# Kernel optimization log

Hardware: AMD Instinct MI355X
Metric: run time of the kernel (lower is better)

Reference implementation:

```python
import jax, jax.numpy as jnp
import numpy as np

K = 6

def _diag_indices(H, W):
    # stable argsort of anti-diagonal index i+j over row-major flattening
    i = np.arange(H)[:, None]
    j = np.arange(W)[None, :]
    order = np.argsort((i + j).ravel(), kind='stable')
    return order, np.argsort(order, kind='stable')

def _selective_scan(u, delta, A, Bs, Cs, D, delta_bias):
    # u, delta: (B,K,D,L); A: (K,D,N); Bs,Cs: (B,K,N,L); D,delta_bias: (K,D)
    delta = jax.nn.softplus(delta + delta_bias[None, :, :, None])
    dA = jnp.exp(jnp.einsum('bkdl,kdn->lbkdn', delta, A))          # (L,B,K,D,N)
    dBu = jnp.einsum('bkdl,bknl,bkdl->lbkdn', delta, Bs, u)         # (L,B,K,D,N)
    Cl = jnp.moveaxis(Cs, -1, 0)                                    # (L,B,K,N)
    x0 = jnp.zeros(dA.shape[1:], dA.dtype)
    def step(x, inp):
        dA_t, dBu_t, C_t = inp
        x = dA_t * x + dBu_t
        y = jnp.einsum('bkdn,bkn->bkd', x, C_t)
        return x, y
    _, ys = jax.lax.scan(step, x0, (dA, dBu, Cl))
    y = jnp.moveaxis(ys, 0, -1)                                     # (B,K,D,L)
    return y + u * D[None, :, :, None]

def reference(x, W_in, conv_w, conv_b, x_proj_w, dt_w, dt_b, A_logs, Ds, ln_g, ln_b, W_out):
    B, H, W, C = x.shape
    L = H * W
    di = dt_w.shape[1]
    dt_rank = dt_w.shape[2]
    N = A_logs.shape[1]
    # in_proj (no bias) and split
    xz = jnp.einsum('bhwc,oc->bhwo', x, W_in)
    xx, z = jnp.split(xz, 2, axis=-1)
    # depthwise conv 3x3, SAME padding, + bias, SiLU
    xc = jnp.transpose(xx, (0, 3, 1, 2))                            # (B,di,H,W)
    xc = jax.lax.conv_general_dilated(xc, conv_w, (1, 1), 'SAME',
            feature_group_count=di, dimension_numbers=('NCHW', 'OIHW', 'NCHW'))
    xc = jax.nn.silu(xc + conv_b[None, :, None, None])
    # build 6 scan orderings
    x_flat = xc.reshape(B, di, L)
    x_t = jnp.transpose(xc, (0, 1, 3, 2)).reshape(B, di, L)
    x_hwwh = jnp.stack([x_flat, x_t], axis=1)                       # (B,2,di,L)
    xs4 = jnp.concatenate([x_hwwh, x_hwwh[..., ::-1]], axis=1)      # (B,4,di,L)
    x_invhh = jnp.flip(xc, axis=-1).reshape(B, di, L)               # flip W only
    x_hh = jnp.stack([x_flat, x_invhh], axis=1)                     # (B,2,di,L)
    diag_idx, rev_idx = _diag_indices(H, W)
    xs = jnp.concatenate([xs4, x_hh[..., diag_idx]], axis=1)        # (B,6,di,L)
    # projections
    x_dbl = jnp.einsum('bkdl,kcd->bkcl', xs, x_proj_w)
    dts, Bs, Cs = jnp.split(x_dbl, [dt_rank, dt_rank + N], axis=2)
    dts = jnp.einsum('bkrl,kdr->bkdl', dts, dt_w)
    A = -jnp.exp(A_logs).reshape(K, di, N)
    out_y = _selective_scan(xs, dts, A, Bs, Cs, Ds.reshape(K, di), dt_b)
    # undo the 6 orderings
    inv_y = out_y[:, 2:4][..., ::-1]
    wh_y = jnp.transpose(out_y[:, 1].reshape(B, di, W, H), (0, 1, 3, 2)).reshape(B, di, L)
    invwh_y = jnp.transpose(inv_y[:, 1].reshape(B, di, W, H), (0, 1, 3, 2)).reshape(B, di, L)
    transhh = out_y[:, 4:6][..., rev_idx]
    invhh = transhh[:, 1][..., ::-1]
    y = out_y[:, 0] + inv_y[:, 0] + wh_y + invwh_y + transhh[:, 0] + invhh  # (B,di,L)
    y = jnp.transpose(y, (0, 2, 1)).reshape(B, H, W, di)
    # LayerNorm (eps=1e-5)
    mu = y.mean(-1, keepdims=True)
    var = ((y - mu) ** 2).mean(-1, keepdims=True)
    y = (y - mu) * jax.lax.rsqrt(var + 1e-5) * ln_g + ln_b
    y = y * jax.nn.silu(z)
    return jnp.einsum('bhwd,od->bhwo', y, W_out)

def setup_inputs():
    key = jax.random.key(0)
    ks = jax.random.split(key, 8)
    d_model, di, N, dt_rank = 64, 128, 16, 4
    x = jax.random.normal(ks[0], (1, 64, 64, d_model), jnp.float32)
    W_in = jax.random.normal(ks[1], (2 * di, d_model), jnp.float32) * d_model ** -0.5
    conv_w = jax.random.normal(ks[2], (di, 1, 3, 3), jnp.float32) / 3.0
    conv_b = jnp.zeros((di,), jnp.float32)
    x_proj_w = jax.random.normal(ks[3], (K, dt_rank + 2 * N, di), jnp.float32) * di ** -0.5
    s = dt_rank ** -0.5
    dt_w = jax.random.uniform(ks[4], (K, di, dt_rank), jnp.float32, -s, s)
    dt = jnp.exp(jax.random.uniform(ks[5], (K, di), jnp.float32)
                 * (np.log(0.1) - np.log(0.001)) + np.log(0.001))
    dt = jnp.clip(dt, 1e-4)
    dt_b = dt + jnp.log(-jnp.expm1(-dt))
    A_logs = jnp.log(jnp.tile(jnp.arange(1, N + 1, dtype=jnp.float32)[None, :], (K * di, 1)))
    Ds = jnp.ones((K * di,), jnp.float32)
    ln_g = jnp.ones((di,), jnp.float32)
    ln_b = jnp.zeros((di,), jnp.float32)
    W_out = jax.random.normal(ks[6], (d_model, di), jnp.float32) * di ** -0.5
    return {"x": x, "W_in": W_in, "conv_w": conv_w, "conv_b": conv_b,
            "x_proj_w": x_proj_w, "dt_w": dt_w, "dt_b": dt_b, "A_logs": A_logs,
            "Ds": Ds, "ln_g": ln_g, "ln_b": ln_b, "W_out": W_out}
```

## Files before the change

kernel.cpp:

```cpp
#include <hip/hip_runtime.h>
#include <math.h>

#define L    4096
#define DI   128
#define NS   16
#define KK   6
#define DTR  4
#define CM   64
#define NC   256
#define CH   (L/NC)

__device__ __forceinline__ float softplus_f(float x){
    return x > 20.f ? x : __logf(1.f + __expf(x));
}
__device__ __forceinline__ float silu_f(float x){
    return x / (1.f + __expf(-x));
}

__device__ __forceinline__ int rankp(int p){
    int h = p >> 6, w = p & 63, s = h + w;
    int imin = s > 63 ? s - 63 : 0;
    int off = (s < 64) ? (s*(s+1))/2 : 4096 - ((127-s)*(128-s))/2;
    return off + (h - imin);
}

__device__ __forceinline__ int perm_in(int k, int l, const int* __restrict__ diag){
    switch(k){
        case 0: return l;
        case 1: return ((l&63)<<6) | (l>>6);
        case 2: return (L-1) - l;
        case 3: { int m = (L-1)-l; return ((m&63)<<6) | (m>>6); }
        case 4: return diag[l];
        default: return diag[l] ^ 63;
    }
}

__global__ __launch_bounds__(256) void k_init(const float* __restrict__ W_in,
                                              const float* __restrict__ W_out,
                                              int* __restrict__ diag_idx,
                                              float* __restrict__ WI4,
                                              float* __restrict__ WO4){
    int t = blockIdx.x*256 + threadIdx.x;
    diag_idx[rankp(t)] = t;
    {
        int d4 = t >> 8, o = t & 255;
        float4 v = make_float4(W_in[(size_t)o*CM + d4*4+0], W_in[(size_t)o*CM + d4*4+1],
                               W_in[(size_t)o*CM + d4*4+2], W_in[(size_t)o*CM + d4*4+3]);
        ((float4*)WI4)[d4*256 + o] = v;
    }
    if(t < 2048){
        int d4 = t >> 6, o = t & 63;
        float4 v = make_float4(W_out[(size_t)o*DI + d4*4+0], W_out[(size_t)o*DI + d4*4+1],
                               W_out[(size_t)o*DI + d4*4+2], W_out[(size_t)o*DI + d4*4+3]);
        ((float4*)WO4)[d4*64 + o] = v;
    }
}

__global__ __launch_bounds__(256) void k_inproj(const float* __restrict__ x,
                                                const float* __restrict__ WI4,
                                                float* __restrict__ xx_t,
                                                float* __restrict__ sz){
    int pb = blockIdx.x * 8;
    int o  = threadIdx.x;
    __shared__ float xr[8][CM];
    if(o < 128) ((float4*)&xr[0][0])[o] = ((const float4*)(x + (size_t)pb*CM))[o];
    float4 w[16];
    const float4* W4 = (const float4*)WI4;
    #pragma unroll
    for(int q=0;q<16;q++) w[q] = W4[q*256 + o];
    __syncthreads();
    float acc[8];
    #pragma unroll
    for(int pi=0;pi<8;pi++) acc[pi] = 0.f;
    #pragma unroll
    for(int q=0;q<16;q++){
        float4 wv = w[q];
        #pragma unroll
        for(int pi=0;pi<8;pi++){
            float4 xv = *((const float4*)&xr[pi][q*4]);
            acc[pi] += wv.x*xv.x + wv.y*xv.y + wv.z*xv.z + wv.w*xv.w;
        }
    }
    #pragma unroll
    for(int pi=0;pi<8;pi++){
        int p = pb + pi;
        if(o < DI) xx_t[(size_t)p*DI + o] = acc[pi];
        else       sz[(size_t)p*DI + (o-DI)] = silu_f(acc[pi]);
    }
}

__global__ __launch_bounds__(256) void k_conv(const float* __restrict__ xx_t,
                                              const float* __restrict__ cw,
                                              const float* __restrict__ cb,
                                              float* __restrict__ xc_t){
    int idx = blockIdx.x*256 + threadIdx.x;
    int d = idx & 127, p = idx >> 7;
    int h = p >> 6, w = p & 63;
    float acc = cb[d];
    #pragma unroll
    for(int dh=-1; dh<=1; dh++){
        int hh = h+dh; if(hh < 0 || hh >= 64) continue;
        #pragma unroll
        for(int dw=-1; dw<=1; dw++){
            int ww = w+dw; if(ww < 0 || ww >= 64) continue;
            acc += cw[d*9 + (dh+1)*3+(dw+1)] * xx_t[(size_t)(hh*64+ww)*DI + d];
        }
    }
    xc_t[idx] = silu_f(acc);
}

#define XT_S 132
__global__ __launch_bounds__(256) void k_proj(const float* __restrict__ xc_t,
                                              const float* __restrict__ xpw,
                                              const int* __restrict__ diag,
                                              float* __restrict__ dts,
                                              float* __restrict__ BT,
                                              float* __restrict__ CT){
    int k  = blockIdx.x >> 6;
    int l0 = (blockIdx.x & 63) * 64;
    int t  = threadIdx.x;
    __shared__ float xt[64*XT_S];
    #pragma unroll
    for(int q=0;q<8;q++){
        int lin = q*256 + t;
        int row = lin >> 5, col4 = lin & 31;
        int p = perm_in(k, l0+row, diag);
        float4 v = ((const float4*)(xc_t + (size_t)p*DI))[col4];
        *((float4*)(xt + row*XT_S + col4*4)) = v;
    }
    __syncthreads();
    int l = t & 63, c0 = (t>>6)*9;
    const float* xr = xt + l*XT_S;
    float acc[9];
    #pragma unroll
    for(int j=0;j<9;j++) acc[j] = 0.f;
    const float4* wbase = (const float4*)(xpw + (size_t)k*36*DI);
    for(int dd4=0; dd4<32; dd4++){
        float4 xv = *((const float4*)(xr + dd4*4));
        #pragma unroll
        for(int j=0;j<9;j++){
            float4 wv = wbase[(c0+j)*32 + dd4];
            acc[j] += wv.x*xv.x + wv.y*xv.y + wv.z*xv.z + wv.w*xv.w;
        }
    }
    #pragma unroll
    for(int j=0;j<9;j++){
        int c = c0 + j;
        if(c < 4)        dts[((size_t)k*4 + c)*L + l0 + l] = acc[j];
        else if(c < 20)  BT[((size_t)k*L + l0 + l)*NS + (c-4)]  = acc[j];
        else             CT[((size_t)k*L + l0 + l)*NS + (c-20)] = acc[j];
    }
}

__global__ __launch_bounds__(128) void k_scan1(const float* __restrict__ xc_t,
                                               const float* __restrict__ dts,
                                               const float* __restrict__ BT,
                                               const float* __restrict__ dtw,
                                               const float* __restrict__ dtb,
                                               const float* __restrict__ A_logs,
                                               const int* __restrict__ diag,
                                               float* __restrict__ apb,
                                               float* __restrict__ xlb){
    int bk = blockIdx.x;
    int k = bk >> 8, cc = bk & (NC-1);
    int d = threadIdx.x;
    int l0 = cc*CH;

    __shared__ float Bt[CH*NS];
    __shared__ float dtt[4*CH];
    __shared__ int   pt[CH];

    if(d < 64) ((float4*)Bt)[d] = ((const float4*)(BT + ((size_t)k*L + l0)*NS))[d];
    else { int j = d-64; int r = j>>4, i = j&15;
           dtt[j] = dts[((size_t)k*4 + r)*L + l0 + i]; }
    if(d < CH) pt[d] = perm_in(k, l0+d, diag);
    __syncthreads();

    float u[CH];
    #pragma unroll
    for(int i=0;i<CH;i++) u[i] = xc_t[(size_t)pt[i]*DI + d];

    float4 w4 = ((const float4*)dtw)[(size_t)k*DI + d];
    float  bb = dtb[k*DI + d];
    float A[NS];
    {
        const float4* ar = (const float4*)(A_logs + ((size_t)k*DI + d)*NS);
        #pragma unroll
        for(int q=0;q<4;q++){
            float4 a4 = ar[q];
            A[q*4+0] = -__expf(a4.x); A[q*4+1] = -__expf(a4.y);
            A[q*4+2] = -__expf(a4.z); A[q*4+3] = -__expf(a4.w);
        }
    }
    float x[NS], ap[NS];
    #pragma unroll
    for(int n=0;n<NS;n++){ x[n] = 0.f; ap[n] = 1.f; }

    #pragma unroll
    for(int i=0;i<CH;i++){
        float dv = bb + w4.x*dtt[i] + w4.y*dtt[CH+i] + w4.z*dtt[2*CH+i] + w4.w*dtt[3*CH+i];
        float delta = softplus_f(dv);
        float du = delta*u[i];
        const float* Bi = Bt + i*NS;
        #pragma unroll
        for(int n=0;n<NS;n++){
            float da = __expf(delta*A[n]);
            x[n] = da*x[n] + du*Bi[n];
            ap[n] *= da;
        }
    }
    float* apd = apb + ((size_t)bk*DI + d)*NS;
    float* xld = xlb + ((size_t)bk*DI + d)*NS;
    #pragma unroll
    for(int q=0;q<4;q++){
        ((float4*)apd)[q] = make_float4(ap[q*4],ap[q*4+1],ap[q*4+2],ap[q*4+3]);
        ((float4*)xld)[q] = make_float4(x[q*4], x[q*4+1], x[q*4+2], x[q*4+3]);
    }
}

__global__ __launch_bounds__(512) void k_comb(float* __restrict__ apb,
                                              const float* __restrict__ xlb){
    int k    = blockIdx.x >> 5;
    int gidx = blockIdx.x & 31;
    int seg  = threadIdx.x >> 6;
    int c    = threadIdx.x & 63;
    int rem  = gidx*64 + c;
    size_t sb = (size_t)k*NC*2048 + (size_t)seg*32*2048 + rem;
    float a[32], xl[32];
    #pragma unroll
    for(int j=0;j<32;j++){
        a[j]  = apb[sb + (size_t)j*2048];
        xl[j] = xlb[sb + (size_t)j*2048];
    }
    float Aag = 1.f, Xag = 0.f;
    #pragma unroll
    for(int j=0;j<32;j++){ Xag = a[j]*Xag + xl[j]; Aag *= a[j]; }
    __shared__ float sA[64][8], sX[64][8];
    sA[c][seg] = Aag; sX[c][seg] = Xag;
    __syncthreads();
    if(threadIdx.x < 64){
        float run = 0.f;
        #pragma unroll
        for(int s=0;s<8;s++){
            float at = sA[c][s], xt = sX[c][s];
            sX[c][s] = run;
            run = at*run + xt;
        }
    }
    __syncthreads();
    float run = sX[c][seg];
    #pragma unroll
    for(int j=0;j<32;j++){
        apb[sb + (size_t)j*2048] = run;
        run = a[j]*run + xl[j];
    }
}

__global__ __launch_bounds__(128) void k_scan2(const float* __restrict__ xc_t,
                                               const float* __restrict__ dts,
                                               const float* __restrict__ BT,
                                               const float* __restrict__ CT,
                                               const float* __restrict__ dtw,
                                               const float* __restrict__ dtb,
                                               const float* __restrict__ A_logs,
                                               const float* __restrict__ Dsv,
                                               const int* __restrict__ diag,
                                               const float* __restrict__ inib,
                                               float* __restrict__ yk){
    int bk = blockIdx.x;
    int k = bk >> 8, cc = bk & (NC-1);
    int d = threadIdx.x;
    int l0 = cc*CH;

    __shared__ float Bt[CH*NS];
    __shared__ float Ct[CH*NS];
    __shared__ float dtt[4*CH];
    __shared__ int   pt[CH];

    if(d < 64){
        ((float4*)Bt)[d] = ((const float4*)(BT + ((size_t)k*L + l0)*NS))[d];
        int r = d>>4, i = d&15;
        dtt[d] = dts[((size_t)k*4 + r)*L + l0 + i];
    } else {
        ((float4*)Ct)[d-64] = ((const float4*)(CT + ((size_t)k*L + l0)*NS))[d-64];
    }
    if(d < CH) pt[d] = perm_in(k, l0+d, diag);
    __syncthreads();

    float u[CH];
    #pragma unroll
    for(int i=0;i<CH;i++) u[i] = xc_t[(size_t)pt[i]*DI + d];

    float4 w4 = ((const float4*)dtw)[(size_t)k*DI + d];
    float  bb = dtb[k*DI + d];
    float  Dv = Dsv[k*DI + d];
    float A[NS];
    {
        const float4* ar = (const float4*)(A_logs + ((size_t)k*DI + d)*NS);
        #pragma unroll
        for(int q=0;q<4;q++){
            float4 a4 = ar[q];
            A[q*4+0] = -__expf(a4.x); A[q*4+1] = -__expf(a4.y);
            A[q*4+2] = -__expf(a4.z); A[q*4+3] = -__expf(a4.w);
        }
    }
    float x[NS];
    {
        const float4* ir = (const float4*)(inib + ((size_t)bk*DI + d)*NS);
        #pragma unroll
        for(int q=0;q<4;q++){
            float4 v = ir[q];
            x[q*4+0]=v.x; x[q*4+1]=v.y; x[q*4+2]=v.z; x[q*4+3]=v.w;
        }
    }

    #pragma unroll
    for(int i=0;i<CH;i++){
        float dv = bb + w4.x*dtt[i] + w4.y*dtt[CH+i] + w4.z*dtt[2*CH+i] + w4.w*dtt[3*CH+i];
        float delta = softplus_f(dv);
        float du = delta*u[i];
        const float* Bi = Bt + i*NS;
        const float* Ci = Ct + i*NS;
        float y = 0.f;
        #pragma unroll
        for(int n=0;n<NS;n++){
            float da = __expf(delta*A[n]);
            x[n] = da*x[n] + du*Bi[n];
            y += x[n]*Ci[n];
        }
        yk[((size_t)k*L + l0 + i)*DI + d] = y + u[i]*Dv;
    }
}

__global__ __launch_bounds__(128) void k_out(const float* __restrict__ yk,
                                             const float* __restrict__ sz,
                                             const float* __restrict__ ln_g,
                                             const float* __restrict__ ln_b,
                                             const float* __restrict__ WO4,
                                             float* __restrict__ out){
    int pb = blockIdx.x*4;
    int d = threadIdx.x;
    __shared__ float ms[4][DI];
    __shared__ float red[4][2][2];
    float g = ln_g[d], bc = ln_b[d];
    float yv[4];
    #pragma unroll
    for(int pi=0;pi<4;pi++){
        int p = pb+pi;
        int tp = ((p&63)<<6) | (p>>6);
        float y;
        y  = yk[((size_t)0*L + p)*DI + d];
        y += yk[((size_t)1*L + tp)*DI + d];
        y += yk[((size_t)2*L + (L-1-p))*DI + d];
        y += yk[((size_t)3*L + (L-1-tp))*DI + d];
        y += yk[((size_t)4*L + rankp(p))*DI + d];
        y += yk[((size_t)5*L + rankp(L-1-p))*DI + d];
        yv[pi] = y;
        float s1 = y, s2 = y*y;
        #pragma unroll
        for(int m=1;m<64;m<<=1){ s1 += __shfl_xor(s1,m,64); s2 += __shfl_xor(s2,m,64); }
        if((d&63)==0){ red[pi][d>>6][0] = s1; red[pi][d>>6][1] = s2; }
    }
    __syncthreads();
    #pragma unroll
    for(int pi=0;pi<4;pi++){
        float mu  = (red[pi][0][0]+red[pi][1][0]) * (1.f/DI);
        float var = (red[pi][0][1]+red[pi][1][1]) * (1.f/DI) - mu*mu;
        float yh = (yv[pi]-mu)*rsqrtf(var+1e-5f)*g + bc;
        ms[pi][d] = yh * sz[(size_t)(pb+pi)*DI + d];
    }
    __syncthreads();
    int o = d & 63, w = d >> 6;
    const float4* W4 = (const float4*)WO4;
    float acc[2];
    acc[0] = 0.f; acc[1] = 0.f;
    #pragma unroll 8
    for(int d4=0; d4<32; d4++){
        float4 wv = W4[d4*64 + o];
        #pragma unroll
        for(int q=0;q<2;q++){
            float4 xv = *((const float4*)&ms[w*2+q][d4*4]);
            acc[q] += wv.x*xv.x + wv.y*xv.y + wv.z*xv.z + wv.w*xv.w;
        }
    }
    #pragma unroll
    for(int q=0;q<2;q++)
        out[(size_t)(pb + w*2 + q)*CM + o] = acc[q];
}

extern "C" void kernel_launch(void* const* d_in, const int* in_sizes, int n_in,
                              void* d_out, int out_size, void* d_ws, size_t ws_size,
                              hipStream_t stream) {
    const float* x      = (const float*)d_in[0];
    const float* W_in   = (const float*)d_in[1];
    const float* conv_w = (const float*)d_in[2];
    const float* conv_b = (const float*)d_in[3];
    const float* xpw    = (const float*)d_in[4];
    const float* dtw    = (const float*)d_in[5];
    const float* dtb    = (const float*)d_in[6];
    const float* A_logs = (const float*)d_in[7];
    const float* Dsv    = (const float*)d_in[8];
    const float* ln_g   = (const float*)d_in[9];
    const float* ln_b   = (const float*)d_in[10];
    const float* W_out  = (const float*)d_in[11];
    float* out = (float*)d_out;

    float* ws = (float*)d_ws;
    float* xx_t = ws;
    float* sz   = xx_t + (size_t)L*DI;
    float* xc_t = sz   + (size_t)L*DI;
    float* dts  = xc_t + (size_t)L*DI;
    float* BT   = dts  + (size_t)KK*4*L;
    float* CT   = BT   + (size_t)KK*L*NS;
    float* apb  = CT   + (size_t)KK*L*NS;
    float* xlb  = apb  + (size_t)KK*NC*DI*NS;
    float* yk   = xlb  + (size_t)KK*NC*DI*NS;
    int*   diag = (int*)(yk + (size_t)KK*L*DI);
    float* WI4  = (float*)(diag + L);
    float* WO4  = WI4 + (size_t)16*256*4;

    k_init  <<<L/256, 256, 0, stream>>>(W_in, W_out, diag, WI4, WO4);
    k_inproj<<<L/8, 256, 0, stream>>>(x, WI4, xx_t, sz);
    k_conv  <<<(L*DI)/256, 256, 0, stream>>>(xx_t, conv_w, conv_b, xc_t);
    k_proj  <<<KK*64, 256, 0, stream>>>(xc_t, xpw, diag, dts, BT, CT);
    k_scan1 <<<KK*NC, 128, 0, stream>>>(xc_t, dts, BT, dtw, dtb, A_logs, diag, apb, xlb);
    k_comb  <<<KK*32, 512, 0, stream>>>(apb, xlb);
    k_scan2 <<<KK*NC, 128, 0, stream>>>(xc_t, dts, BT, CT, dtw, dtb, A_logs, Dsv, diag, apb, yk);
    k_out   <<<L/4, 128, 0, stream>>>(yk, sz, ln_g, ln_b, WO4, out);
}
```

Measured before the change: 175.5 us.

## Fuse x_proj into first scan pass and vectorize depthwise conv

The projection kernel and the first chunked-scan pass are merged into one kernel. Each 128-thread block loads a 32-row permuted tile of activations into shared memory, computes dt/B/C for it, and then runs the chunk-local scan for two 16-step chunks straight from shared memory. This removes one launch and the global re-read of the permuted inputs, dts and B. The depthwise conv now processes four channels per thread with float4 loads, using a transposed weight layout that is prepared in the init kernel. In exchange the fused kernel has fewer threads per block for the projection GEMV, and that part may get less parallelism.

```diff
diff --git a/kernel.cpp b/kernel.cpp
--- a/kernel.cpp
+++ b/kernel.cpp
@@ -5,10 +5,9 @@
 #define DI   128
 #define NS   16
 #define KK   6
-#define DTR  4
 #define CM   64
 #define NC   256
-#define CH   (L/NC)
+#define CH   16
 
 __device__ __forceinline__ float softplus_f(float x){
     return x > 20.f ? x : __logf(1.f + __expf(x));
@@ -37,22 +36,28 @@
 
 __global__ __launch_bounds__(256) void k_init(const float* __restrict__ W_in,
                                               const float* __restrict__ W_out,
+                                              const float* __restrict__ conv_w,
                                               int* __restrict__ diag_idx,
                                               float* __restrict__ WI4,
-                                              float* __restrict__ WO4){
+                                              float* __restrict__ WO4,
+                                              float* __restrict__ cwT){
     int t = blockIdx.x*256 + threadIdx.x;
     diag_idx[rankp(t)] = t;
     {
         int d4 = t >> 8, o = t & 255;
-        float4 v = make_float4(W_in[(size_t)o*CM + d4*4+0], W_in[(size_t)o*CM + d4*4+1],
-                               W_in[(size_t)o*CM + d4*4+2], W_in[(size_t)o*CM + d4*4+3]);
-        ((float4*)WI4)[d4*256 + o] = v;
+        ((float4*)WI4)[d4*256 + o] = make_float4(
+            W_in[(size_t)o*CM + d4*4+0], W_in[(size_t)o*CM + d4*4+1],
+            W_in[(size_t)o*CM + d4*4+2], W_in[(size_t)o*CM + d4*4+3]);
     }
     if(t < 2048){
         int d4 = t >> 6, o = t & 63;
-        float4 v = make_float4(W_out[(size_t)o*DI + d4*4+0], W_out[(size_t)o*DI + d4*4+1],
-                               W_out[(size_t)o*DI + d4*4+2], W_out[(size_t)o*DI + d4*4+3]);
-        ((float4*)WO4)[d4*64 + o] = v;
+        ((float4*)WO4)[d4*64 + o] = make_float4(
+            W_out[(size_t)o*DI + d4*4+0], W_out[(size_t)o*DI + d4*4+1],
+            W_out[(size_t)o*DI + d4*4+2], W_out[(size_t)o*DI + d4*4+3]);
+    }
+    if(t < 9*DI){
+        int tap = t >> 7, d = t & 127;
+        cwT[t] = conv_w[d*9 + tap];
     }
 }
 
@@ -90,96 +95,92 @@
 }
 
 __global__ __launch_bounds__(256) void k_conv(const float* __restrict__ xx_t,
-                                              const float* __restrict__ cw,
+                                              const float* __restrict__ cwT,
                                               const float* __restrict__ cb,
                                               float* __restrict__ xc_t){
     int idx = blockIdx.x*256 + threadIdx.x;
-    int d = idx & 127, p = idx >> 7;
+    int dq = (idx & 31)*4, p = idx >> 5;
     int h = p >> 6, w = p & 63;
-    float acc = cb[d];
+    float4 acc = *((const float4*)(cb + dq));
     #pragma unroll
     for(int dh=-1; dh<=1; dh++){
         int hh = h+dh; if(hh < 0 || hh >= 64) continue;
         #pragma unroll
         for(int dw=-1; dw<=1; dw++){
             int ww = w+dw; if(ww < 0 || ww >= 64) continue;
-            acc += cw[d*9 + (dh+1)*3+(dw+1)] * xx_t[(size_t)(hh*64+ww)*DI + d];
-        }
-    }
-    xc_t[idx] = silu_f(acc);
+            int tap = (dh+1)*3 + (dw+1);
+            float4 xv = *((const float4*)(xx_t + (size_t)(hh*64+ww)*DI + dq));
+            float4 wv = *((const float4*)(cwT + tap*DI + dq));
+            acc.x += wv.x*xv.x; acc.y += wv.y*xv.y;
+            acc.z += wv.z*xv.z; acc.w += wv.w*xv.w;
+        }
+    }
+    *((float4*)(xc_t + (size_t)p*DI + dq)) =
+        make_float4(silu_f(acc.x), silu_f(acc.y), silu_f(acc.z), silu_f(acc.w));
 }
 
 #define XT_S 132
-__global__ __launch_bounds__(256) void k_proj(const float* __restrict__ xc_t,
-                                              const float* __restrict__ xpw,
-                                              const int* __restrict__ diag,
-                                              float* __restrict__ dts,
-                                              float* __restrict__ BT,
-                                              float* __restrict__ CT){
-    int k  = blockIdx.x >> 6;
-    int l0 = (blockIdx.x & 63) * 64;
-    int t  = threadIdx.x;
-    __shared__ float xt[64*XT_S];
+__global__ __launch_bounds__(128) void k_projscan(const float* __restrict__ xc_t,
+                                                  const float* __restrict__ xpw,
+                                                  const int* __restrict__ diag,
+                                                  const float* __restrict__ dtw,
+                                                  const float* __restrict__ dtb,
+                                                  const float* __restrict__ A_logs,
+                                                  float* __restrict__ dts,
+                                                  float* __restrict__ BT,
+                                                  float* __restrict__ CT,
+                                                  float* __restrict__ apb,
+                                                  float* __restrict__ xlb){
+    int b = blockIdx.x;
+    int k = b >> 7, tile = b & 127;
+    int l0 = tile * 32;
+    int t = threadIdx.x;
+    __shared__ float xt[32*XT_S];
+    __shared__ float Btl[32*NS];
+    __shared__ float dtt[4*32];
+
     #pragma unroll
     for(int q=0;q<8;q++){
-        int lin = q*256 + t;
+        int lin = q*128 + t;
         int row = lin >> 5, col4 = lin & 31;
         int p = perm_in(k, l0+row, diag);
         float4 v = ((const float4*)(xc_t + (size_t)p*DI))[col4];
         *((float4*)(xt + row*XT_S + col4*4)) = v;
     }
     __syncthreads();
-    int l = t & 63, c0 = (t>>6)*9;
-    const float* xr = xt + l*XT_S;
-    float acc[9];
-    #pragma unroll
-    for(int j=0;j<9;j++) acc[j] = 0.f;
-    const float4* wbase = (const float4*)(xpw + (size_t)k*36*DI);
-    for(int dd4=0; dd4<32; dd4++){
-        float4 xv = *((const float4*)(xr + dd4*4));
+
+    {
+        int l = t & 31, c0 = (t>>5)*9;
+        const float* xr = xt + l*XT_S;
+        float acc[9];
+        #pragma unroll
+        for(int j=0;j<9;j++) acc[j] = 0.f;
+        const float4* wbase = (const float4*)(xpw + (size_t)k*36*DI);
+        for(int dd4=0; dd4<32; dd4++){
+            float4 xv = *((const float4*)(xr + dd4*4));
+            #pragma unroll
+            for(int j=0;j<9;j++){
+                float4 wv = wbase[(c0+j)*32 + dd4];
+                acc[j] += wv.x*xv.x + wv.y*xv.y + wv.z*xv.z + wv.w*xv.w;
+            }
+        }
         #pragma unroll
         for(int j=0;j<9;j++){
-            float4 wv = wbase[(c0+j)*32 + dd4];
-            acc[j] += wv.x*xv.x + wv.y*xv.y + wv.z*xv.z + wv.w*xv.w;
-        }
-    }
-    #pragma unroll
-    for(int j=0;j<9;j++){
-        int c = c0 + j;
-        if(c < 4)        dts[((size_t)k*4 + c)*L + l0 + l] = acc[j];
-        else if(c < 20)  BT[((size_t)k*L + l0 + l)*NS + (c-4)]  = acc[j];
-        else             CT[((size_t)k*L + l0 + l)*NS + (c-20)] = acc[j];
-    }
-}
-
-__global__ __launch_bounds__(128) void k_scan1(const float* __restrict__ xc_t,
-                                               const float* __restrict__ dts,
-                                               const float* __restrict__ BT,
-                                               const float* __restrict__ dtw,
-                                               const float* __restrict__ dtb,
-                                               const float* __restrict__ A_logs,
-                                               const int* __restrict__ diag,
-                                               float* __restrict__ apb,
-                                               float* __restrict__ xlb){
-    int bk = blockIdx.x;
-    int k = bk >> 8, cc = bk & (NC-1);
-    int d = threadIdx.x;
-    int l0 = cc*CH;
-
-    __shared__ float Bt[CH*NS];
-    __shared__ float dtt[4*CH];
-    __shared__ int   pt[CH];
-
-    if(d < 64) ((float4*)Bt)[d] = ((const float4*)(BT + ((size_t)k*L + l0)*NS))[d];
-    else { int j = d-64; int r = j>>4, i = j&15;
-           dtt[j] = dts[((size_t)k*4 + r)*L + l0 + i]; }
-    if(d < CH) pt[d] = perm_in(k, l0+d, diag);
-    __syncthreads();
-
-    float u[CH];
-    #pragma unroll
-    for(int i=0;i<CH;i++) u[i] = xc_t[(size_t)pt[i]*DI + d];
-
+            int c = c0 + j;
+            if(c < 4){
+                dts[((size_t)k*4 + c)*L + l0 + l] = acc[j];
+                dtt[c*32 + l] = acc[j];
+            } else if(c < 20){
+                BT[((size_t)k*L + l0 + l)*NS + (c-4)] = acc[j];
+                Btl[l*NS + (c-4)] = acc[j];
+            } else {
+                CT[((size_t)k*L + l0 + l)*NS + (c-20)] = acc[j];
+            }
+        }
+    }
+    __syncthreads();
+
+    int d = t;
     float4 w4 = ((const float4*)dtw)[(size_t)k*DI + d];
     float  bb = dtb[k*DI + d];
     float A[NS];
@@ -192,29 +193,33 @@
             A[q*4+2] = -__expf(a4.z); A[q*4+3] = -__expf(a4.w);
         }
     }
-    float x[NS], ap[NS];
-    #pragma unroll
-    for(int n=0;n<NS;n++){ x[n] = 0.f; ap[n] = 1.f; }
-
-    #pragma unroll
-    for(int i=0;i<CH;i++){
-        float dv = bb + w4.x*dtt[i] + w4.y*dtt[CH+i] + w4.z*dtt[2*CH+i] + w4.w*dtt[3*CH+i];
-        float delta = softplus_f(dv);
-        float du = delta*u[i];
-        const float* Bi = Bt + i*NS;
-        #pragma unroll
-        for(int n=0;n<NS;n++){
-            float da = __expf(delta*A[n]);
-            x[n] = da*x[n] + du*Bi[n];
-            ap[n] *= da;
-        }
-    }
-    float* apd = apb + ((size_t)bk*DI + d)*NS;
-    float* xld = xlb + ((size_t)bk*DI + d)*NS;
-    #pragma unroll
-    for(int q=0;q<4;q++){
-        ((float4*)apd)[q] = make_float4(ap[q*4],ap[q*4+1],ap[q*4+2],ap[q*4+3]);
-        ((float4*)xld)[q] = make_float4(x[q*4], x[q*4+1], x[q*4+2], x[q*4+3]);
+    for(int q=0;q<2;q++){
+        float xs[NS], ap[NS];
+        #pragma unroll
+        for(int n=0;n<NS;n++){ xs[n] = 0.f; ap[n] = 1.f; }
+        #pragma unroll
+        for(int i=0;i<CH;i++){
+            int l = q*CH + i;
+            float u = xt[l*XT_S + d];
+            float dv = bb + w4.x*dtt[l] + w4.y*dtt[32+l] + w4.z*dtt[64+l] + w4.w*dtt[96+l];
+            float delta = softplus_f(dv);
+            float du = delta*u;
+            const float* Bi = Btl + l*NS;
+            #pragma unroll
+            for(int n=0;n<NS;n++){
+                float da = __expf(delta*A[n]);
+                xs[n] = da*xs[n] + du*Bi[n];
+                ap[n] *= da;
+            }
+        }
+        int bk = k*NC + tile*2 + q;
+        float* apd = apb + ((size_t)bk*DI + d)*NS;
+        float* xld = xlb + ((size_t)bk*DI + d)*NS;
+        #pragma unroll
+        for(int qq=0;qq<4;qq++){
+            ((float4*)apd)[qq] = make_float4(ap[qq*4],ap[qq*4+1],ap[qq*4+2],ap[qq*4+3]);
+            ((float4*)xld)[qq] = make_float4(xs[qq*4],xs[qq*4+1],xs[qq*4+2],xs[qq*4+3]);
+        }
     }
 }
 
@@ -271,12 +276,10 @@
     int k = bk >> 8, cc = bk & (NC-1);
     int d = threadIdx.x;
     int l0 = cc*CH;
-
     __shared__ float Bt[CH*NS];
     __shared__ float Ct[CH*NS];
     __shared__ float dtt[4*CH];
     __shared__ int   pt[CH];
-
     if(d < 64){
         ((float4*)Bt)[d] = ((const float4*)(BT + ((size_t)k*L + l0)*NS))[d];
         int r = d>>4, i = d&15;
@@ -286,11 +289,9 @@
     }
     if(d < CH) pt[d] = perm_in(k, l0+d, diag);
     __syncthreads();
-
     float u[CH];
     #pragma unroll
     for(int i=0;i<CH;i++) u[i] = xc_t[(size_t)pt[i]*DI + d];
-
     float4 w4 = ((const float4*)dtw)[(size_t)k*DI + d];
     float  bb = dtb[k*DI + d];
     float  Dv = Dsv[k*DI + d];
@@ -304,16 +305,15 @@
             A[q*4+2] = -__expf(a4.z); A[q*4+3] = -__expf(a4.w);
         }
     }
-    float x[NS];
+    float xv[NS];
     {
         const float4* ir = (const float4*)(inib + ((size_t)bk*DI + d)*NS);
         #pragma unroll
         for(int q=0;q<4;q++){
             float4 v = ir[q];
-            x[q*4+0]=v.x; x[q*4+1]=v.y; x[q*4+2]=v.z; x[q*4+3]=v.w;
-        }
-    }
-
+            xv[q*4+0]=v.x; xv[q*4+1]=v.y; xv[q*4+2]=v.z; xv[q*4+3]=v.w;
+        }
+    }
     #pragma unroll
     for(int i=0;i<CH;i++){
         float dv = bb + w4.x*dtt[i] + w4.y*dtt[CH+i] + w4.z*dtt[2*CH+i] + w4.w*dtt[3*CH+i];
@@ -325,8 +325,8 @@
         #pragma unroll
         for(int n=0;n<NS;n++){
             float da = __expf(delta*A[n]);
-            x[n] = da*x[n] + du*Bi[n];
-            y += x[n]*Ci[n];
+            xv[n] = da*xv[n] + du*Bi[n];
+            y += xv[n]*Ci[n];
         }
         yk[((size_t)k*L + l0 + i)*DI + d] = y + u[i]*Dv;
     }
@@ -418,13 +418,14 @@
     int*   diag = (int*)(yk + (size_t)KK*L*DI);
     float* WI4  = (float*)(diag + L);
     float* WO4  = WI4 + (size_t)16*256*4;
-
-    k_init  <<<L/256, 256, 0, stream>>>(W_in, W_out, diag, WI4, WO4);
-    k_inproj<<<L/8, 256, 0, stream>>>(x, WI4, xx_t, sz);
-    k_conv  <<<(L*DI)/256, 256, 0, stream>>>(xx_t, conv_w, conv_b, xc_t);
-    k_proj  <<<KK*64, 256, 0, stream>>>(xc_t, xpw, diag, dts, BT, CT);
-    k_scan1 <<<KK*NC, 128, 0, stream>>>(xc_t, dts, BT, dtw, dtb, A_logs, diag, apb, xlb);
-    k_comb  <<<KK*32, 512, 0, stream>>>(apb, xlb);
-    k_scan2 <<<KK*NC, 128, 0, stream>>>(xc_t, dts, BT, CT, dtw, dtb, A_logs, Dsv, diag, apb, yk);
-    k_out   <<<L/4, 128, 0, stream>>>(yk, sz, ln_g, ln_b, WO4, out);
-}
+    float* cwT  = WO4 + (size_t)32*64*4;
+
+    k_init    <<<L/256, 256, 0, stream>>>(W_in, W_out, conv_w, diag, WI4, WO4, cwT);
+    k_inproj  <<<L/8, 256, 0, stream>>>(x, WI4, xx_t, sz);
+    k_conv    <<<(L*DI/4)/256, 256, 0, stream>>>(xx_t, cwT, conv_b, xc_t);
+    k_projscan<<<KK*128, 128, 0, stream>>>(xc_t, xpw, diag, dtw, dtb, A_logs,
+                                           dts, BT, CT, apb, xlb);
+    k_comb    <<<KK*32, 512, 0, stream>>>(apb, xlb);
+    k_scan2   <<<KK*NC, 128, 0, stream>>>(xc_t, dts, BT, CT, dtw, dtb, A_logs, Dsv, diag, apb, yk);
+    k_out     <<<L/4, 128, 0, stream>>>(yk, sz, ln_g, ln_b, WO4, out);
+}
```

New measurement: 182.1 us. 1.04x slower.

## Double scan chunk length and vectorize depthwise conv with transposed weights

Applied to the files above, without the earlier changes.

Halves the number of scan chunks (chunk length 16 to 32), so scan1/scan2 launch half as many blocks, each doing longer sequential work, and the chunk-combine kernel processes 16 chunks per segment instead of 32. The depthwise conv now handles four channels per thread with float4 loads, using a tap-major weight copy built in the init kernel. This cuts combine traffic and per-block setup and gives wider conv memory accesses, at the cost of fewer blocks and a longer serial dependency chain in each scan block.

```diff
diff --git a/kernel.cpp b/kernel.cpp
--- a/kernel.cpp
+++ b/kernel.cpp
@@ -5,10 +5,9 @@
 #define DI   128
 #define NS   16
 #define KK   6
-#define DTR  4
 #define CM   64
-#define NC   256
-#define CH   (L/NC)
+#define NC   128
+#define CH   32
 
 __device__ __forceinline__ float softplus_f(float x){
     return x > 20.f ? x : __logf(1.f + __expf(x));
@@ -37,22 +36,28 @@
 
 __global__ __launch_bounds__(256) void k_init(const float* __restrict__ W_in,
                                               const float* __restrict__ W_out,
+                                              const float* __restrict__ conv_w,
                                               int* __restrict__ diag_idx,
                                               float* __restrict__ WI4,
-                                              float* __restrict__ WO4){
+                                              float* __restrict__ WO4,
+                                              float* __restrict__ cwT){
     int t = blockIdx.x*256 + threadIdx.x;
     diag_idx[rankp(t)] = t;
     {
         int d4 = t >> 8, o = t & 255;
-        float4 v = make_float4(W_in[(size_t)o*CM + d4*4+0], W_in[(size_t)o*CM + d4*4+1],
-                               W_in[(size_t)o*CM + d4*4+2], W_in[(size_t)o*CM + d4*4+3]);
-        ((float4*)WI4)[d4*256 + o] = v;
+        ((float4*)WI4)[d4*256 + o] = make_float4(
+            W_in[(size_t)o*CM + d4*4+0], W_in[(size_t)o*CM + d4*4+1],
+            W_in[(size_t)o*CM + d4*4+2], W_in[(size_t)o*CM + d4*4+3]);
     }
     if(t < 2048){
         int d4 = t >> 6, o = t & 63;
-        float4 v = make_float4(W_out[(size_t)o*DI + d4*4+0], W_out[(size_t)o*DI + d4*4+1],
-                               W_out[(size_t)o*DI + d4*4+2], W_out[(size_t)o*DI + d4*4+3]);
-        ((float4*)WO4)[d4*64 + o] = v;
+        ((float4*)WO4)[d4*64 + o] = make_float4(
+            W_out[(size_t)o*DI + d4*4+0], W_out[(size_t)o*DI + d4*4+1],
+            W_out[(size_t)o*DI + d4*4+2], W_out[(size_t)o*DI + d4*4+3]);
+    }
+    if(t < 9*DI){
+        int tap = t >> 7, d = t & 127;
+        cwT[t] = conv_w[d*9 + tap];
     }
 }
 
@@ -90,23 +95,28 @@
 }
 
 __global__ __launch_bounds__(256) void k_conv(const float* __restrict__ xx_t,
-                                              const float* __restrict__ cw,
+                                              const float* __restrict__ cwT,
                                               const float* __restrict__ cb,
                                               float* __restrict__ xc_t){
     int idx = blockIdx.x*256 + threadIdx.x;
-    int d = idx & 127, p = idx >> 7;
+    int dq = (idx & 31)*4, p = idx >> 5;
     int h = p >> 6, w = p & 63;
-    float acc = cb[d];
+    float4 acc = *((const float4*)(cb + dq));
     #pragma unroll
     for(int dh=-1; dh<=1; dh++){
         int hh = h+dh; if(hh < 0 || hh >= 64) continue;
         #pragma unroll
         for(int dw=-1; dw<=1; dw++){
             int ww = w+dw; if(ww < 0 || ww >= 64) continue;
-            acc += cw[d*9 + (dh+1)*3+(dw+1)] * xx_t[(size_t)(hh*64+ww)*DI + d];
-        }
-    }
-    xc_t[idx] = silu_f(acc);
+            int tap = (dh+1)*3 + (dw+1);
+            float4 xv = *((const float4*)(xx_t + (size_t)(hh*64+ww)*DI + dq));
+            float4 wv = *((const float4*)(cwT + tap*DI + dq));
+            acc.x += wv.x*xv.x; acc.y += wv.y*xv.y;
+            acc.z += wv.z*xv.z; acc.w += wv.w*xv.w;
+        }
+    }
+    *((float4*)(xc_t + (size_t)p*DI + dq)) =
+        make_float4(silu_f(acc.x), silu_f(acc.y), silu_f(acc.z), silu_f(acc.w));
 }
 
 #define XT_S 132
@@ -162,7 +172,7 @@
                                                float* __restrict__ apb,
                                                float* __restrict__ xlb){
     int bk = blockIdx.x;
-    int k = bk >> 8, cc = bk & (NC-1);
+    int k = bk >> 7, cc = bk & (NC-1);
     int d = threadIdx.x;
     int l0 = cc*CH;
 
@@ -170,9 +180,8 @@
     __shared__ float dtt[4*CH];
     __shared__ int   pt[CH];
 
-    if(d < 64) ((float4*)Bt)[d] = ((const float4*)(BT + ((size_t)k*L + l0)*NS))[d];
-    else { int j = d-64; int r = j>>4, i = j&15;
-           dtt[j] = dts[((size_t)k*4 + r)*L + l0 + i]; }
+    ((float4*)Bt)[d] = ((const float4*)(BT + ((size_t)k*L + l0)*NS))[d];
+    dtt[d] = dts[((size_t)k*4 + (d>>5))*L + l0 + (d&31)];
     if(d < CH) pt[d] = perm_in(k, l0+d, diag);
     __syncthreads();
 
@@ -192,9 +201,9 @@
             A[q*4+2] = -__expf(a4.z); A[q*4+3] = -__expf(a4.w);
         }
     }
-    float x[NS], ap[NS];
-    #pragma unroll
-    for(int n=0;n<NS;n++){ x[n] = 0.f; ap[n] = 1.f; }
+    float xv[NS], ap[NS];
+    #pragma unroll
+    for(int n=0;n<NS;n++){ xv[n] = 0.f; ap[n] = 1.f; }
 
     #pragma unroll
     for(int i=0;i<CH;i++){
@@ -205,7 +214,7 @@
         #pragma unroll
         for(int n=0;n<NS;n++){
             float da = __expf(delta*A[n]);
-            x[n] = da*x[n] + du*Bi[n];
+            xv[n] = da*xv[n] + du*Bi[n];
             ap[n] *= da;
         }
     }
@@ -214,7 +223,7 @@
     #pragma unroll
     for(int q=0;q<4;q++){
         ((float4*)apd)[q] = make_float4(ap[q*4],ap[q*4+1],ap[q*4+2],ap[q*4+3]);
-        ((float4*)xld)[q] = make_float4(x[q*4], x[q*4+1], x[q*4+2], x[q*4+3]);
+        ((float4*)xld)[q] = make_float4(xv[q*4],xv[q*4+1],xv[q*4+2],xv[q*4+3]);
     }
 }
 
@@ -225,16 +234,16 @@
     int seg  = threadIdx.x >> 6;
     int c    = threadIdx.x & 63;
     int rem  = gidx*64 + c;
-    size_t sb = (size_t)k*NC*2048 + (size_t)seg*32*2048 + rem;
-    float a[32], xl[32];
-    #pragma unroll
-    for(int j=0;j<32;j++){
+    size_t sb = (size_t)k*NC*2048 + (size_t)seg*16*2048 + rem;
+    float a[16], xl[16];
+    #pragma unroll
+    for(int j=0;j<16;j++){
         a[j]  = apb[sb + (size_t)j*2048];
         xl[j] = xlb[sb + (size_t)j*2048];
     }
     float Aag = 1.f, Xag = 0.f;
     #pragma unroll
-    for(int j=0;j<32;j++){ Xag = a[j]*Xag + xl[j]; Aag *= a[j]; }
+    for(int j=0;j<16;j++){ Xag = a[j]*Xag + xl[j]; Aag *= a[j]; }
     __shared__ float sA[64][8], sX[64][8];
     sA[c][seg] = Aag; sX[c][seg] = Xag;
     __syncthreads();
@@ -250,7 +259,7 @@
     __syncthreads();
     float run = sX[c][seg];
     #pragma unroll
-    for(int j=0;j<32;j++){
+    for(int j=0;j<16;j++){
         apb[sb + (size_t)j*2048] = run;
         run = a[j]*run + xl[j];
     }
@@ -268,7 +277,7 @@
                                                const float* __restrict__ inib,
                                                float* __restrict__ yk){
     int bk = blockIdx.x;
-    int k = bk >> 8, cc = bk & (NC-1);
+    int k = bk >> 7, cc = bk & (NC-1);
     int d = threadIdx.x;
     int l0 = cc*CH;
 
@@ -277,13 +286,9 @@
     __shared__ float dtt[4*CH];
     __shared__ int   pt[CH];
 
-    if(d < 64){
-        ((float4*)Bt)[d] = ((const float4*)(BT + ((size_t)k*L + l0)*NS))[d];
-        int r = d>>4, i = d&15;
-        dtt[d] = dts[((size_t)k*4 + r)*L + l0 + i];
-    } else {
-        ((float4*)Ct)[d-64] = ((const float4*)(CT + ((size_t)k*L + l0)*NS))[d-64];
-    }
+    ((float4*)Bt)[d] = ((const float4*)(BT + ((size_t)k*L + l0)*NS))[d];
+    ((float4*)Ct)[d] = ((const float4*)(CT + ((size_t)k*L + l0)*NS))[d];
+    dtt[d] = dts[((size_t)k*4 + (d>>5))*L + l0 + (d&31)];
     if(d < CH) pt[d] = perm_in(k, l0+d, diag);
     __syncthreads();
 
@@ -304,13 +309,13 @@
             A[q*4+2] = -__expf(a4.z); A[q*4+3] = -__expf(a4.w);
         }
     }
-    float x[NS];
+    float xv[NS];
     {
         const float4* ir = (const float4*)(inib + ((size_t)bk*DI + d)*NS);
         #pragma unroll
         for(int q=0;q<4;q++){
             float4 v = ir[q];
-            x[q*4+0]=v.x; x[q*4+1]=v.y; x[q*4+2]=v.z; x[q*4+3]=v.w;
+            xv[q*4+0]=v.x; xv[q*4+1]=v.y; xv[q*4+2]=v.z; xv[q*4+3]=v.w;
         }
     }
 
@@ -325,8 +330,8 @@
         #pragma unroll
         for(int n=0;n<NS;n++){
             float da = __expf(delta*A[n]);
-            x[n] = da*x[n] + du*Bi[n];
-            y += x[n]*Ci[n];
+            xv[n] = da*xv[n] + du*Bi[n];
+            y += xv[n]*Ci[n];
         }
         yk[((size_t)k*L + l0 + i)*DI + d] = y + u[i]*Dv;
     }
@@ -418,10 +423,11 @@
     int*   diag = (int*)(yk + (size_t)KK*L*DI);
     float* WI4  = (float*)(diag + L);
     float* WO4  = WI4 + (size_t)16*256*4;
-
-    k_init  <<<L/256, 256, 0, stream>>>(W_in, W_out, diag, WI4, WO4);
+    float* cwT  = WO4 + (size_t)32*64*4;
+
+    k_init  <<<L/256, 256, 0, stream>>>(W_in, W_out, conv_w, diag, WI4, WO4, cwT);
     k_inproj<<<L/8, 256, 0, stream>>>(x, WI4, xx_t, sz);
-    k_conv  <<<(L*DI)/256, 256, 0, stream>>>(xx_t, conv_w, conv_b, xc_t);
+    k_conv  <<<(L*DI/4)/256, 256, 0, stream>>>(xx_t, cwT, conv_b, xc_t);
     k_proj  <<<KK*64, 256, 0, stream>>>(xc_t, xpw, diag, dts, BT, CT);
     k_scan1 <<<KK*NC, 128, 0, stream>>>(xc_t, dts, BT, dtw, dtb, A_logs, diag, apb, xlb);
     k_comb  <<<KK*32, 512, 0, stream>>>(apb, xlb);
```

Result: slower. 188.5 us (+7.4%).
